# Kernel optimization log

Measured on AMD Instinct MI355X. Metric: run time of the kernel, lower is better.

Reference implementation:

```python
import jax, jax.numpy as jnp
import numpy as np

B, QN, KN, DIN, DPROJ = 8, 2048, 2048, 1024, 1024

def setup_inputs() -> dict:
    key = jax.random.key(0)
    ks = jax.random.split(key, 10)
    s = 1.0 / np.sqrt(DIN)
    return {
        "query": jax.random.normal(ks[0], (B, QN, DIN), jnp.float32),
        "key": jax.random.normal(ks[1], (B, KN, DIN), jnp.float32),
        "value": jax.random.normal(ks[2], (B, KN, DIN), jnp.float32),
        "mask": jax.random.randint(ks[3], (B, KN), 0, 2, jnp.int32),
        "Wq": jax.random.uniform(ks[4], (DPROJ, DIN), jnp.float32, -s, s),
        "bq": jax.random.uniform(ks[5], (DPROJ,), jnp.float32, -s, s),
        "Wk": jax.random.uniform(ks[6], (DPROJ, DIN), jnp.float32, -s, s),
        "bk": jax.random.uniform(ks[7], (DPROJ,), jnp.float32, -s, s),
        "Wv": jax.random.uniform(ks[8], (DPROJ, DIN), jnp.float32, -s, s),
        "bv": jax.random.uniform(ks[9], (DPROJ,), jnp.float32, -s, s),
    }

def reference(query, key, value, mask, Wq, bq, Wk, bk, Wv, bv):
    pq = jnp.einsum('bqc,dc->bqd', query, Wq) + bq  # (b, qn, dproj)
    pk = jnp.einsum('bkc,dc->bkd', key, Wk) + bk    # (b, kn, dproj)
    pv = jnp.einsum('bkc,dc->bkd', value, Wv) + bv  # (b, kn, dproj)
    scores = jnp.einsum('bqd,bkd->bqk', pq, pk) / jnp.sqrt(jnp.float32(DPROJ))
    m = mask[:, None, :]  # (b, 1, kn) broadcasts over qn
    scores = jnp.where(m == 0, jnp.float32(-1e9), scores)
    attn = jax.nn.softmax(scores, axis=-1)
    attn = attn * m.astype(attn.dtype)  # post-softmax double mask
    ctx = jnp.einsum('bqk,bkd->bqd', attn, pv)
    return (ctx, attn)
```

## Files before the change

### kernel.cpp

```cpp
#include <hip/hip_runtime.h>
#include <hip/hip_bf16.h>


typedef __bf16 bf16;
typedef __bf16 bf16x4 __attribute__((ext_vector_type(4)));
typedef __bf16 bf16x8 __attribute__((ext_vector_type(8)));
typedef float f32x4 __attribute__((ext_vector_type(4)));

#define TILE 128
#define BK 32

__device__ __forceinline__ void gld_lds16(const bf16* g, bf16* l) {
  __builtin_amdgcn_global_load_lds(
      (const __attribute__((address_space(1))) void*)g,
      (__attribute__((address_space(3))) void*)l, 16, 0, 0);
}

__global__ __launch_bounds__(256, 2)
void gemm_f32in(const float* __restrict__ A, int lda,
                const float* __restrict__ Bt, int ldb,
                bf16* __restrict__ C, int ldc,
                const float* __restrict__ bias, int bias_mode, int K)
{
  __shared__ bf16 As[TILE * BK];
  __shared__ bf16 Bs[TILE * BK];
  const int tid = threadIdx.x;
  const int wave = tid >> 6, lane = tid & 63;
  const int wm = (wave >> 1) * 64, wn = (wave & 1) * 64;
  const long m0 = (long)blockIdx.x * TILE;
  const long n0 = (long)blockIdx.y * TILE;

  f32x4 acc[4][4] = {};
  const int fr = lane & 15, fq = lane >> 4;

  for (int k0 = 0; k0 < K; k0 += BK) {
    __syncthreads();
#pragma unroll
    for (int j = 0; j < 4; ++j) {
      int c = j * 256 + tid;
      int row = c >> 3, col = (c & 7) * 4;
      f32x4 av = *(const f32x4*)&A[(m0 + row) * (long)lda + k0 + col];
      f32x4 bv = *(const f32x4*)&Bt[(n0 + row) * (long)ldb + k0 + col];
      bf16x4 ab, bb;
      ab[0] = (bf16)av[0]; ab[1] = (bf16)av[1]; ab[2] = (bf16)av[2]; ab[3] = (bf16)av[3];
      bb[0] = (bf16)bv[0]; bb[1] = (bf16)bv[1]; bb[2] = (bf16)bv[2]; bb[3] = (bf16)bv[3];
      *(bf16x4*)&As[row * BK + col] = ab;
      *(bf16x4*)&Bs[row * BK + col] = bb;
    }
    __syncthreads();

    bf16x8 af[4], bg[4];
#pragma unroll
    for (int i = 0; i < 4; ++i)
      af[i] = *(const bf16x8*)&As[(wm + i * 16 + fr) * BK + fq * 8];
#pragma unroll
    for (int i = 0; i < 4; ++i)
      bg[i] = *(const bf16x8*)&Bs[(wn + i * 16 + fr) * BK + fq * 8];
#pragma unroll
    for (int mi = 0; mi < 4; ++mi)
#pragma unroll
      for (int ni = 0; ni < 4; ++ni)
        acc[mi][ni] = __builtin_amdgcn_mfma_f32_16x16x32_bf16(
            af[mi], bg[ni], acc[mi][ni], 0, 0, 0);
  }

  const int cc = lane & 15, cq = lane >> 4;
#pragma unroll
  for (int mi = 0; mi < 4; ++mi)
#pragma unroll
    for (int ni = 0; ni < 4; ++ni)
#pragma unroll
      for (int r = 0; r < 4; ++r) {
        int row = wm + mi * 16 + cq * 4 + r;
        int col = wn + ni * 16 + cc;
        float v = acc[mi][ni][r];
        if (bias_mode == 1) v += bias[n0 + col];
        else if (bias_mode == 2) v += bias[m0 + row];
        C[(m0 + row) * (long)ldc + (n0 + col)] = (bf16)v;
      }
}

__global__ __launch_bounds__(256, 2)
void gemm_bf16(const bf16* __restrict__ A, int lda, long sA,
               const bf16* __restrict__ Bt, int ldb, long sB,
               float* __restrict__ C, int ldc, long sC,
               int K, float scale)
{
  __shared__ bf16 As[TILE * BK];
  __shared__ bf16 Bs[TILE * BK];
  const int tid = threadIdx.x;
  const int wave = tid >> 6, lane = tid & 63;
  const int wm = (wave >> 1) * 64, wn = (wave & 1) * 64;
  const long m0 = (long)blockIdx.x * TILE;
  const long n0 = (long)blockIdx.y * TILE;
  A  += (long)blockIdx.z * sA;
  Bt += (long)blockIdx.z * sB;
  C  += (long)blockIdx.z * sC;

  f32x4 acc[4][4] = {};

  const int srow = tid >> 2;
  const int scol = (tid & 3) * 8;
  const bf16* Ag0 = A  + (m0 + srow) * (long)lda + scol;
  const bf16* Ag1 = A  + (m0 + 64 + srow) * (long)lda + scol;
  const bf16* Bg0 = Bt + (n0 + srow) * (long)ldb + scol;
  const bf16* Bg1 = Bt + (n0 + 64 + srow) * (long)ldb + scol;
  bf16* Al0 = &As[tid * 8];
  bf16* Al1 = &As[(256 + tid) * 8];
  bf16* Bl0 = &Bs[tid * 8];
  bf16* Bl1 = &Bs[(256 + tid) * 8];

  const int fr = lane & 15, fq = lane >> 4;

  for (int k0 = 0; k0 < K; k0 += BK) {
    __syncthreads();
    gld_lds16(Ag0 + k0, Al0);
    gld_lds16(Ag1 + k0, Al1);
    gld_lds16(Bg0 + k0, Bl0);
    gld_lds16(Bg1 + k0, Bl1);
    __syncthreads();

    bf16x8 af[4], bg[4];
#pragma unroll
    for (int i = 0; i < 4; ++i)
      af[i] = *(const bf16x8*)&As[(wm + i * 16 + fr) * BK + fq * 8];
#pragma unroll
    for (int i = 0; i < 4; ++i)
      bg[i] = *(const bf16x8*)&Bs[(wn + i * 16 + fr) * BK + fq * 8];
#pragma unroll
    for (int mi = 0; mi < 4; ++mi)
#pragma unroll
      for (int ni = 0; ni < 4; ++ni)
        acc[mi][ni] = __builtin_amdgcn_mfma_f32_16x16x32_bf16(
            af[mi], bg[ni], acc[mi][ni], 0, 0, 0);
  }

  const int cc = lane & 15, cq = lane >> 4;
#pragma unroll
  for (int mi = 0; mi < 4; ++mi)
#pragma unroll
    for (int ni = 0; ni < 4; ++ni)
#pragma unroll
      for (int r = 0; r < 4; ++r) {
        int row = wm + mi * 16 + cq * 4 + r;
        int col = wn + ni * 16 + cc;
        C[(m0 + row) * (long)ldc + (n0 + col)] = acc[mi][ni][r] * scale;
      }
}

__global__ __launch_bounds__(256)
void softmax_mask(const int* __restrict__ mask, float* __restrict__ attn,
                  bf16* __restrict__ attnb)
{
  const int row = blockIdx.x;
  const int b = row >> 11;
  float* arow = attn + (long)row * 2048;
  bf16* brow = attnb + (long)row * 2048;
  const int* mrow = mask + (b << 11);
  const int tid = threadIdx.x;
  const int lane = tid & 63, wave = tid >> 6;

  f32x4 s[2];
  int4 mk[2];
  s[0] = *(const f32x4*)&arow[tid * 4];
  s[1] = *(const f32x4*)&arow[1024 + tid * 4];
  mk[0] = *(const int4*)&mrow[tid * 4];
  mk[1] = *(const int4*)&mrow[1024 + tid * 4];
  const int m[8] = {mk[0].x, mk[0].y, mk[0].z, mk[0].w,
                    mk[1].x, mk[1].y, mk[1].z, mk[1].w};

  float mx = -3e38f;
#pragma unroll
  for (int i = 0; i < 8; ++i)
    if (m[i]) mx = fmaxf(mx, s[i >> 2][i & 3]);
#pragma unroll
  for (int off = 32; off > 0; off >>= 1) mx = fmaxf(mx, __shfl_xor(mx, off));
  __shared__ float rmax[4], rsum[4];
  if (lane == 0) rmax[wave] = mx;
  __syncthreads();
  mx = fmaxf(fmaxf(rmax[0], rmax[1]), fmaxf(rmax[2], rmax[3]));

  float e[8], sum = 0.f;
#pragma unroll
  for (int i = 0; i < 8; ++i) {
    e[i] = m[i] ? __expf(s[i >> 2][i & 3] - mx) : 0.f;
    sum += e[i];
  }
#pragma unroll
  for (int off = 32; off > 0; off >>= 1) sum += __shfl_xor(sum, off);
  if (lane == 0) rsum[wave] = sum;
  __syncthreads();
  sum = rsum[0] + rsum[1] + rsum[2] + rsum[3];
  float inv = sum > 0.f ? 1.f / sum : 0.f;

  f32x4 o; bf16x4 ob;
#pragma unroll
  for (int h = 0; h < 2; ++h) {
#pragma unroll
    for (int i = 0; i < 4; ++i) {
      float v = e[h * 4 + i] * inv;
      o[i] = v; ob[i] = (bf16)v;
    }
    *(f32x4*)&arow[h * 1024 + tid * 4] = o;
    *(bf16x4*)&brow[h * 1024 + tid * 4] = ob;
  }
}

extern "C" void kernel_launch(void* const* d_in, const int* in_sizes, int n_in,
                              void* d_out, int out_size, void* d_ws, size_t ws_size,
                              hipStream_t stream)
{
  const float* query = (const float*)d_in[0];
  const float* key   = (const float*)d_in[1];
  const float* value = (const float*)d_in[2];
  const int*   mask  = (const int*)d_in[3];
  const float* Wq = (const float*)d_in[4];
  const float* bq = (const float*)d_in[5];
  const float* Wk = (const float*)d_in[6];
  const float* bk = (const float*)d_in[7];
  const float* Wv = (const float*)d_in[8];
  const float* bv = (const float*)d_in[9];

  float* ctx  = (float*)d_out;
  float* attn = ctx + (size_t)8 * 2048 * 1024;

  bf16* Pq    = (bf16*)d_ws;
  bf16* Pk    = Pq + (size_t)16384 * 1024;
  bf16* PvT   = Pk + (size_t)16384 * 1024;
  bf16* attnb = (bf16*)d_ws;

  dim3 blk(256);

  hipLaunchKernelGGL(gemm_f32in, dim3(128, 8), blk, 0, stream,
      query, 1024, Wq, 1024, Pq, 1024, bq, 1, 1024);
  hipLaunchKernelGGL(gemm_f32in, dim3(128, 8), blk, 0, stream,
      key, 1024, Wk, 1024, Pk, 1024, bk, 1, 1024);
  hipLaunchKernelGGL(gemm_f32in, dim3(8, 128), blk, 0, stream,
      Wv, 1024, value, 1024, PvT, 16384, bv, 2, 1024);
  hipLaunchKernelGGL(gemm_bf16, dim3(16, 16, 8), blk, 0, stream,
      Pq, 1024, (long)2048 * 1024, Pk, 1024, (long)2048 * 1024,
      attn, 2048, (long)2048 * 2048, 1024, 0.03125f);
  hipLaunchKernelGGL(softmax_mask, dim3(16384), blk, 0, stream, mask, attn, attnb);
  hipLaunchKernelGGL(gemm_bf16, dim3(16, 8, 8), blk, 0, stream,
      attnb, 2048, (long)2048 * 2048, PvT, 16384, 2048L,
      ctx, 1024, (long)2048 * 1024, 2048, 1.0f);
}
```

Baseline: 762.3 us.

## Pre-convert fp32 inputs to bf16 and unify GEMMs with async LDS loads

Adds a standalone fp32-to-bf16 conversion pass for activations and weights, so all projection GEMMs can use the bf16 kernel with direct global-to-LDS loads instead of per-tile fp32 loads and in-register conversion. The GEMM kernels are merged into one template with optional bias and output type, and block traversal now walks the N dimension fastest. This adds an extra read/write pass over roughly 200MB of inputs and more workspace in exchange for a leaner GEMM inner loop.

Result: no change. 770.3 us (+1.0%).

```diff
diff --git a/kernel.cpp b/kernel.cpp
--- a/kernel.cpp
+++ b/kernel.cpp
@@ -16,83 +16,34 @@
       (__attribute__((address_space(3))) void*)l, 16, 0, 0);
 }
 
+__global__ __launch_bounds__(256)
+void cvt_f32_bf16(const float* __restrict__ src, bf16* __restrict__ dst, int n4)
+{
+  int i = blockIdx.x * 256 + threadIdx.x;
+  const int stride = gridDim.x * 256;
+  for (; i < n4; i += stride) {
+    f32x4 v = *(const f32x4*)&src[(long)i * 4];
+    bf16x4 o;
+    o[0] = (bf16)v[0]; o[1] = (bf16)v[1]; o[2] = (bf16)v[2]; o[3] = (bf16)v[3];
+    *(bf16x4*)&dst[(long)i * 4] = o;
+  }
+}
+
+template <typename OutT>
 __global__ __launch_bounds__(256, 2)
-void gemm_f32in(const float* __restrict__ A, int lda,
-                const float* __restrict__ Bt, int ldb,
-                bf16* __restrict__ C, int ldc,
-                const float* __restrict__ bias, int bias_mode, int K)
+void gemm_bt(const bf16* __restrict__ A, int lda, long sA,
+             const bf16* __restrict__ Bt, int ldb, long sB,
+             OutT* __restrict__ C, int ldc, long sC,
+             const float* __restrict__ bias, int bias_mode,
+             int K, float scale)
 {
   __shared__ bf16 As[TILE * BK];
   __shared__ bf16 Bs[TILE * BK];
   const int tid = threadIdx.x;
   const int wave = tid >> 6, lane = tid & 63;
   const int wm = (wave >> 1) * 64, wn = (wave & 1) * 64;
-  const long m0 = (long)blockIdx.x * TILE;
-  const long n0 = (long)blockIdx.y * TILE;
-
-  f32x4 acc[4][4] = {};
-  const int fr = lane & 15, fq = lane >> 4;
-
-  for (int k0 = 0; k0 < K; k0 += BK) {
-    __syncthreads();
-#pragma unroll
-    for (int j = 0; j < 4; ++j) {
-      int c = j * 256 + tid;
-      int row = c >> 3, col = (c & 7) * 4;
-      f32x4 av = *(const f32x4*)&A[(m0 + row) * (long)lda + k0 + col];
-      f32x4 bv = *(const f32x4*)&Bt[(n0 + row) * (long)ldb + k0 + col];
-      bf16x4 ab, bb;
-      ab[0] = (bf16)av[0]; ab[1] = (bf16)av[1]; ab[2] = (bf16)av[2]; ab[3] = (bf16)av[3];
-      bb[0] = (bf16)bv[0]; bb[1] = (bf16)bv[1]; bb[2] = (bf16)bv[2]; bb[3] = (bf16)bv[3];
-      *(bf16x4*)&As[row * BK + col] = ab;
-      *(bf16x4*)&Bs[row * BK + col] = bb;
-    }
-    __syncthreads();
-
-    bf16x8 af[4], bg[4];
-#pragma unroll
-    for (int i = 0; i < 4; ++i)
-      af[i] = *(const bf16x8*)&As[(wm + i * 16 + fr) * BK + fq * 8];
-#pragma unroll
-    for (int i = 0; i < 4; ++i)
-      bg[i] = *(const bf16x8*)&Bs[(wn + i * 16 + fr) * BK + fq * 8];
-#pragma unroll
-    for (int mi = 0; mi < 4; ++mi)
-#pragma unroll
-      for (int ni = 0; ni < 4; ++ni)
-        acc[mi][ni] = __builtin_amdgcn_mfma_f32_16x16x32_bf16(
-            af[mi], bg[ni], acc[mi][ni], 0, 0, 0);
-  }
-
-  const int cc = lane & 15, cq = lane >> 4;
-#pragma unroll
-  for (int mi = 0; mi < 4; ++mi)
-#pragma unroll
-    for (int ni = 0; ni < 4; ++ni)
-#pragma unroll
-      for (int r = 0; r < 4; ++r) {
-        int row = wm + mi * 16 + cq * 4 + r;
-        int col = wn + ni * 16 + cc;
-        float v = acc[mi][ni][r];
-        if (bias_mode == 1) v += bias[n0 + col];
-        else if (bias_mode == 2) v += bias[m0 + row];
-        C[(m0 + row) * (long)ldc + (n0 + col)] = (bf16)v;
-      }
-}
-
-__global__ __launch_bounds__(256, 2)
-void gemm_bf16(const bf16* __restrict__ A, int lda, long sA,
-               const bf16* __restrict__ Bt, int ldb, long sB,
-               float* __restrict__ C, int ldc, long sC,
-               int K, float scale)
-{
-  __shared__ bf16 As[TILE * BK];
-  __shared__ bf16 Bs[TILE * BK];
-  const int tid = threadIdx.x;
-  const int wave = tid >> 6, lane = tid & 63;
-  const int wm = (wave >> 1) * 64, wn = (wave & 1) * 64;
-  const long m0 = (long)blockIdx.x * TILE;
-  const long n0 = (long)blockIdx.y * TILE;
+  const long n0 = (long)blockIdx.x * TILE;
+  const long m0 = (long)blockIdx.y * TILE;
   A  += (long)blockIdx.z * sA;
   Bt += (long)blockIdx.z * sB;
   C  += (long)blockIdx.z * sC;
@@ -144,7 +95,10 @@
       for (int r = 0; r < 4; ++r) {
         int row = wm + mi * 16 + cq * 4 + r;
         int col = wn + ni * 16 + cc;
-        C[(m0 + row) * (long)ldc + (n0 + col)] = acc[mi][ni][r] * scale;
+        float v = acc[mi][ni][r] * scale;
+        if (bias_mode == 1) v += bias[n0 + col];
+        else if (bias_mode == 2) v += bias[m0 + row];
+        C[(m0 + row) * (long)ldc + (n0 + col)] = (OutT)v;
       }
 }
 
@@ -224,24 +178,40 @@
   float* ctx  = (float*)d_out;
   float* attn = ctx + (size_t)8 * 2048 * 1024;
 
-  bf16* Pq    = (bf16*)d_ws;
-  bf16* Pk    = Pq + (size_t)16384 * 1024;
-  bf16* PvT   = Pk + (size_t)16384 * 1024;
-  bf16* attnb = (bf16*)d_ws;
+  const size_t NQ = (size_t)16384 * 1024;
+  const size_t NW = (size_t)1024 * 1024;
+
+  bf16* qb   = (bf16*)d_ws;
+  bf16* kb   = qb + NQ;
+  bf16* vb   = kb + NQ;
+  bf16* Wqb  = vb + NQ;
+  bf16* Wkb  = Wqb + NW;
+  bf16* Wvb  = Wkb + NW;
+  bf16* Pq   = Wvb + NW;
+  bf16* Pk   = Pq + NQ;
+  bf16* PvT  = Pk + NQ;
+  bf16* attnb = qb;
 
   dim3 blk(256);
 
-  hipLaunchKernelGGL(gemm_f32in, dim3(128, 8), blk, 0, stream,
-      query, 1024, Wq, 1024, Pq, 1024, bq, 1, 1024);
-  hipLaunchKernelGGL(gemm_f32in, dim3(128, 8), blk, 0, stream,
-      key, 1024, Wk, 1024, Pk, 1024, bk, 1, 1024);
-  hipLaunchKernelGGL(gemm_f32in, dim3(8, 128), blk, 0, stream,
-      Wv, 1024, value, 1024, PvT, 16384, bv, 2, 1024);
-  hipLaunchKernelGGL(gemm_bf16, dim3(16, 16, 8), blk, 0, stream,
+  hipLaunchKernelGGL(cvt_f32_bf16, dim3(4096), blk, 0, stream, query, qb, (int)(NQ / 4));
+  hipLaunchKernelGGL(cvt_f32_bf16, dim3(4096), blk, 0, stream, key,   kb, (int)(NQ / 4));
+  hipLaunchKernelGGL(cvt_f32_bf16, dim3(4096), blk, 0, stream, value, vb, (int)(NQ / 4));
+  hipLaunchKernelGGL(cvt_f32_bf16, dim3(1024), blk, 0, stream, Wq, Wqb, (int)(NW / 4));
+  hipLaunchKernelGGL(cvt_f32_bf16, dim3(1024), blk, 0, stream, Wk, Wkb, (int)(NW / 4));
+  hipLaunchKernelGGL(cvt_f32_bf16, dim3(1024), blk, 0, stream, Wv, Wvb, (int)(NW / 4));
+
+  hipLaunchKernelGGL(gemm_bt<bf16>, dim3(8, 128, 1), blk, 0, stream,
+      qb, 1024, 0L, Wqb, 1024, 0L, Pq, 1024, 0L, bq, 1, 1024, 1.0f);
+  hipLaunchKernelGGL(gemm_bt<bf16>, dim3(8, 128, 1), blk, 0, stream,
+      kb, 1024, 0L, Wkb, 1024, 0L, Pk, 1024, 0L, bk, 1, 1024, 1.0f);
+  hipLaunchKernelGGL(gemm_bt<bf16>, dim3(128, 8, 1), blk, 0, stream,
+      Wvb, 1024, 0L, vb, 1024, 0L, PvT, 16384, 0L, bv, 2, 1024, 1.0f);
+  hipLaunchKernelGGL(gemm_bt<float>, dim3(16, 16, 8), blk, 0, stream,
       Pq, 1024, (long)2048 * 1024, Pk, 1024, (long)2048 * 1024,
-      attn, 2048, (long)2048 * 2048, 1024, 0.03125f);
+      attn, 2048, (long)2048 * 2048, (const float*)nullptr, 0, 1024, 0.03125f);
   hipLaunchKernelGGL(softmax_mask, dim3(16384), blk, 0, stream, mask, attn, attnb);
-  hipLaunchKernelGGL(gemm_bf16, dim3(16, 8, 8), blk, 0, stream,
+  hipLaunchKernelGGL(gemm_bt<float>, dim3(8, 16, 8), blk, 0, stream,
       attnb, 2048, (long)2048 * 2048, PvT, 16384, 2048L,
-      ctx, 1024, (long)2048 * 1024, 2048, 1.0f);
-}
+      ctx, 1024, (long)2048 * 1024, (const float*)nullptr, 0, 2048, 1.0f);
+}
```
